# Kernel tuning notes

Measured on AMD Instinct MI355X. Metric: run time of the kernel, lower is better.

## Reference

```python
import jax, jax.numpy as jnp
import numpy as np

NUM_HEADS = 16
HEAD_DIM = 64
D_MODEL = NUM_HEADS * HEAD_DIM  # 1024
FEATURE_DIM = 2 * HEAD_DIM      # 128


def setup_inputs() -> dict:
    key = jax.random.key(0)
    ks = jax.random.split(key, 6)
    B, S = 4, 8192
    scale = D_MODEL ** -0.5
    x = jax.random.normal(ks[0], (B, S, D_MODEL), dtype=jnp.float32)
    Wq = jax.random.normal(ks[1], (D_MODEL, D_MODEL), dtype=jnp.float32) * scale
    Wk = jax.random.normal(ks[2], (D_MODEL, D_MODEL), dtype=jnp.float32) * scale
    Wv = jax.random.normal(ks[3], (D_MODEL, D_MODEL), dtype=jnp.float32) * scale
    Wo = jax.random.normal(ks[4], (D_MODEL, D_MODEL), dtype=jnp.float32) * scale
    # random_features buffer: [head_dim, feature_dim], scaled by head_dim**-0.5
    rf = jax.random.normal(ks[5], (HEAD_DIM, FEATURE_DIM), dtype=jnp.float32) * (HEAD_DIM ** -0.5)
    return {"x": x, "Wq": Wq, "Wk": Wk, "Wv": Wv, "Wo": Wo, "rf": rf}


def _phi(x, rf):
    # x: [B, H, S, head_dim] -> [B, H, S, feature_dim]
    proj = jnp.matmul(x, rf)  # [B, H, S, 2*head_dim]
    cos_p, sin_p = jnp.split(proj, 2, axis=-1)
    return jnp.concatenate([jnp.cos(cos_p), jnp.sin(sin_p)], axis=-1) * (FEATURE_DIM ** -0.5)


def reference(x, Wq, Wk, Wv, Wo, rf):
    B, S, _ = x.shape
    def heads(y):  # [B, S, D] -> [B, H, S, head_dim]
        return y.reshape(B, S, NUM_HEADS, HEAD_DIM).transpose(0, 2, 1, 3)
    Q = heads(x @ Wq)
    K = heads(x @ Wk)
    V = heads(x @ Wv)
    Qp = _phi(Q, rf)  # [B, H, S, F]
    Kp = _phi(K, rf)
    KV = jnp.einsum('bhsf,bhsd->bhfd', Kp, V)        # [B, H, F, head_dim]
    QKV = jnp.einsum('bhsf,bhfd->bhsd', Qp, KV)      # [B, H, S, head_dim]
    Z = jnp.einsum('bhsf,bhf->bhs', Qp, Kp.sum(axis=2))[..., None]
    Z = jnp.clip(Z, 1e-6, None)
    out = (QKV / Z).transpose(0, 2, 1, 3).reshape(B, S, D_MODEL)
    return out @ Wo
```

## Files before the change

### kernel.cpp

```cpp
#include <hip/hip_runtime.h>
#include <stdint.h>


#define DEVINL __device__ __forceinline__

typedef float f32x4 __attribute__((ext_vector_type(4)));
typedef __bf16 bf16x8 __attribute__((ext_vector_type(8)));
typedef unsigned short u16;

#define TSTR 136
#define RSTR 72

DEVINL u16 f2bf(float f) {
  union { float f; uint32_t u; } v; v.f = f;
  uint32_t u = v.u;
  u += 0x7fffu + ((u >> 16) & 1u);
  return (u16)(u >> 16);
}
DEVINL float bf2f(u16 h) {
  union { uint32_t u; float f; } v; v.u = ((uint32_t)h) << 16;
  return v.f;
}

#define GLOAD16(gp, lp) __builtin_amdgcn_global_load_lds( \
    (const __attribute__((address_space(1))) unsigned int*)(gp), \
    (__attribute__((address_space(3))) unsigned int*)(lp), 16, 0, 0)

template <int ROWS>
DEVINL void stage_r128(const uint8_t* g, size_t stride, u16* lds, int wave, int lane) {
#pragma unroll
  for (int j = 0; j < ROWS / 32; ++j) {
    int row = wave * (ROWS / 4) + j * 8 + (lane >> 3);
    GLOAD16(g + (size_t)row * stride + (size_t)(lane & 7) * 16,
            (uint8_t*)lds + (size_t)(wave * (ROWS / 4) + j * 8) * 128);
  }
}
template <int ROWS>
DEVINL void stage_r256(const uint8_t* g, size_t stride, u16* lds, int wave, int lane) {
#pragma unroll
  for (int j = 0; j < ROWS / 16; ++j) {
    int row = wave * (ROWS / 4) + j * 4 + (lane >> 4);
    GLOAD16(g + (size_t)row * stride + (size_t)(lane & 15) * 16,
            (uint8_t*)lds + (size_t)(wave * (ROWS / 4) + j * 4) * 256);
  }
}

DEVINL void stage128_sw(const uint8_t* g, size_t stride, u16* lds, int wave, int lane) {
  const int c = (lane & 7) ^ (lane >> 3);
#pragma unroll
  for (int j = 0; j < 4; ++j) {
    int row = wave * 32 + j * 8 + (lane >> 3);
    GLOAD16(g + (size_t)row * stride + (size_t)c * 16,
            (uint8_t*)lds + (size_t)(wave * 32 + j * 8) * 128);
  }
}

DEVINL void mma128_sw(const u16* As, const u16* Bs, f32x4 acc[4][4],
                      int wr, int wc, int lane) {
#pragma unroll
  for (int kk = 0; kk < 2; ++kk) {
    const int cw = kk * 4 + (lane >> 4);
    const int sw = (cw ^ (lane & 7)) * 8;
    bf16x8 a[4], b[4];
#pragma unroll
    for (int m = 0; m < 4; ++m)
      a[m] = *(const bf16x8*)&As[(size_t)(wr * 64 + m * 16 + (lane & 15)) * 64 + sw];
#pragma unroll
    for (int n = 0; n < 4; ++n)
      b[n] = *(const bf16x8*)&Bs[(size_t)(wc * 64 + n * 16 + (lane & 15)) * 64 + sw];
#pragma unroll
    for (int m = 0; m < 4; ++m)
#pragma unroll
      for (int n = 0; n < 4; ++n)
        acc[m][n] = __builtin_amdgcn_mfma_f32_16x16x32_bf16(a[m], b[n], acc[m][n], 0, 0, 0);
  }
}


__global__ __launch_bounds__(256) void cast_x_kernel(
    const float* __restrict__ src, u16* __restrict__ dst, long n4) {
  long i = (long)blockIdx.x * 256 + threadIdx.x;
  const long stride = (long)gridDim.x * 256;
  const float4* s4 = (const float4*)src;
  uint2* d4 = (uint2*)dst;
  for (; i < n4; i += stride) {
    float4 v = s4[i];
    uint2 o;
    o.x = (uint32_t)f2bf(v.x) | ((uint32_t)f2bf(v.y) << 16);
    o.y = (uint32_t)f2bf(v.z) | ((uint32_t)f2bf(v.w) << 16);
    d4[i] = o;
  }
}

__global__ __launch_bounds__(256) void transpose_cast_kernel(
    const float* __restrict__ src, u16* __restrict__ dst, int R, int C) {
  __shared__ float tile[32 * 33];
  const int ntr = R >> 5;
  const int tr = blockIdx.x % ntr, tc = blockIdx.x / ntr;
  const int tid = threadIdx.x;
  {
    int r = tid >> 3, c4 = (tid & 7) * 4;
    float4 v = *(const float4*)&src[(size_t)(tr * 32 + r) * C + tc * 32 + c4];
    tile[r * 33 + c4 + 0] = v.x;
    tile[r * 33 + c4 + 1] = v.y;
    tile[r * 33 + c4 + 2] = v.z;
    tile[r * 33 + c4 + 3] = v.w;
  }
  __syncthreads();
  {
    int c = tid >> 3, r4 = (tid & 7) * 4;
    uint2 o;
    o.x = (uint32_t)f2bf(tile[(r4 + 0) * 33 + c]) |
          ((uint32_t)f2bf(tile[(r4 + 1) * 33 + c]) << 16);
    o.y = (uint32_t)f2bf(tile[(r4 + 2) * 33 + c]) |
          ((uint32_t)f2bf(tile[(r4 + 3) * 33 + c]) << 16);
    *(uint2*)&dst[(size_t)(tc * 32 + c) * R + tr * 32 + r4] = o;
  }
}

__global__ __launch_bounds__(256, 3) void gemm_qkv_phi_kernel(
    const u16* __restrict__ xb, const u16* __restrict__ wT,
    const u16* __restrict__ rfT,
    u16* __restrict__ Qp, u16* __restrict__ KpT, u16* __restrict__ VhT) {
  __shared__ u16 smem[26624];
  u16* As = smem;
  u16* Bs = smem + 8192;
  u16* Rs = smem + 17408;
  const int tid = threadIdx.x, lane = tid & 63, wave = tid >> 6;
  const int wr = wave >> 1, wc = wave & 1;
  const int xcd = blockIdx.x & 7;
  const int i = blockIdx.x >> 3;
  const int g = i >> 6, j = i & 63;
  const int tn = (g % 3) * 8 + (j >> 3);
  const int tm = xcd * 32 + (g / 3) * 8 + (j & 7);
  const int tensor = tn >> 3;

  f32x4 acc[4][4];
#pragma unroll
  for (int m = 0; m < 4; ++m)
#pragma unroll
    for (int n = 0; n < 4; ++n) acc[m][n] = (f32x4){0.f, 0.f, 0.f, 0.f};

  const uint8_t* aB = (const uint8_t*)(xb + (size_t)tm * 128 * 1024);
  const uint8_t* bB = (const uint8_t*)(wT + (size_t)tn * 128 * 1024);
  for (int kt = 0; kt < 16; ++kt) {
    stage128_sw(aB + kt * 128, 2048, As, wave, lane);
    stage128_sw(bB + kt * 128, 2048, Bs, wave, lane);
    __syncthreads();
    mma128_sw(As, Bs, acc, wr, wc, lane);
    __syncthreads();
  }

  const int b = (tm * 128) >> 13;
  const int sblk = (tm * 128) & 8191;

  if (tensor == 2) {
#pragma unroll
    for (int m = 0; m < 4; ++m) {
      int sl = wr * 64 + m * 16 + (lane >> 4) * 4;
#pragma unroll
      for (int n = 0; n < 4; ++n) {
        int cl = wc * 64 + n * 16 + (lane & 15);
#pragma unroll
        for (int r = 0; r < 4; ++r) smem[cl * TSTR + sl + r] = f2bf(acc[m][n][r]);
      }
    }
    __syncthreads();
#pragma unroll
    for (int it = 0; it < 8; ++it) {
      int cl = it * 16 + (tid >> 4);
      int c = (tn & 7) * 128 + cl;
      int h = c >> 6, d = c & 63;
      size_t off = ((size_t)((b * 16 + h) * 64 + d)) * 8192 + sblk + (tid & 15) * 8;
      *(uint4*)&VhT[off] = *(const uint4*)&smem[cl * TSTR + (tid & 15) * 8];
    }
    return;
  }

#pragma unroll
  for (int m = 0; m < 4; ++m) {
    int sl = wr * 64 + m * 16 + (lane >> 4) * 4;
#pragma unroll
    for (int n = 0; n < 4; ++n) {
      int cl = wc * 64 + n * 16 + (lane & 15);
#pragma unroll
      for (int r = 0; r < 4; ++r) smem[(sl + r) * TSTR + cl] = f2bf(acc[m][n][r]);
    }
  }
#pragma unroll
  for (int p4 = 0; p4 < 4; ++p4) {
    int idx = p4 * 256 + tid;
    int f = idx >> 3, c = idx & 7;
    *(uint4*)&Rs[f * RSTR + c * 8] = *(const uint4*)&rfT[f * 64 + c * 8];
  }
  __syncthreads();

  bf16x8 afr[2][2][2];
#pragma unroll
  for (int hh = 0; hh < 2; ++hh)
#pragma unroll
    for (int kk = 0; kk < 2; ++kk) {
      const int ko = kk * 32 + (lane >> 4) * 8;
#pragma unroll
      for (int m = 0; m < 2; ++m)
        afr[hh][kk][m] = *(const bf16x8*)&smem[
            (size_t)(wave * 32 + m * 16 + (lane & 15)) * TSTR + hh * 64 + ko];
    }
  __syncthreads();

  const float SC = 0.088388347648318447f;
#pragma unroll
  for (int hh = 0; hh < 2; ++hh) {
    const int h = (tn & 7) * 2 + hh;
    f32x4 p[2][8];
#pragma unroll
    for (int m = 0; m < 2; ++m)
#pragma unroll
      for (int n = 0; n < 8; ++n) p[m][n] = (f32x4){0.f, 0.f, 0.f, 0.f};
#pragma unroll
    for (int kk = 0; kk < 2; ++kk) {
      const int ko = kk * 32 + (lane >> 4) * 8;
      bf16x8 bb[8];
#pragma unroll
      for (int n = 0; n < 8; ++n)
        bb[n] = *(const bf16x8*)&Rs[(size_t)(n * 16 + (lane & 15)) * RSTR + ko];
#pragma unroll
      for (int m = 0; m < 2; ++m)
#pragma unroll
        for (int n = 0; n < 8; ++n)
          p[m][n] = __builtin_amdgcn_mfma_f32_16x16x32_bf16(afr[hh][kk][m], bb[n], p[m][n], 0, 0, 0);
    }

    if (tensor == 0) {
#pragma unroll
      for (int m = 0; m < 2; ++m)
#pragma unroll
        for (int n = 0; n < 8; ++n) {
          int f = n * 16 + (lane & 15);
          int sl = wave * 32 + m * 16 + (lane >> 4) * 4;
#pragma unroll
          for (int r = 0; r < 4; ++r) {
            float v = ((n < 4) ? __cosf(p[m][n][r]) : __sinf(p[m][n][r])) * SC;
            smem[(sl + r) * TSTR + f] = f2bf(v);
          }
        }
      __syncthreads();
      const size_t base_bh = (size_t)(b * 16 + h) * 8192;
#pragma unroll
      for (int it = 0; it < 8; ++it) {
        int s = it * 16 + (tid >> 4);
        *(uint4*)&Qp[(base_bh + sblk + s) * 128 + (tid & 15) * 8] =
            *(const uint4*)&smem[s * TSTR + (tid & 15) * 8];
      }
    } else {
#pragma unroll
      for (int m = 0; m < 2; ++m)
#pragma unroll
        for (int n = 0; n < 8; ++n) {
          int f = n * 16 + (lane & 15);
          int sl = wave * 32 + m * 16 + (lane >> 4) * 4;
#pragma unroll
          for (int r = 0; r < 4; ++r) {
            float v = ((n < 4) ? __cosf(p[m][n][r]) : __sinf(p[m][n][r])) * SC;
            smem[f * TSTR + sl + r] = f2bf(v);
          }
        }
      __syncthreads();
#pragma unroll
      for (int it = 0; it < 8; ++it) {
        int f = it * 16 + (tid >> 4);
        *(uint4*)&KpT[((size_t)(b * 16 + h) * 128 + f) * 8192 + sblk + (tid & 15) * 8] =
            *(const uint4*)&smem[f * TSTR + (tid & 15) * 8];
      }
    }
    if (hh == 0) __syncthreads();
  }
}

__global__ __launch_bounds__(256) void kv_partial_kernel(
    const u16* __restrict__ KpT, const u16* __restrict__ VhT,
    float* __restrict__ partial) {
  __shared__ u16 smem2[12288];
  __shared__ float ksmem[256];
  u16* As = smem2;
  u16* Bs = smem2 + 8192;
  const int tid = threadIdx.x, lane = tid & 63, wave = tid >> 6;
  const int bh = blockIdx.x >> 4, ch = blockIdx.x & 15;
  const uint8_t* aB = (const uint8_t*)(KpT + (size_t)bh * 128 * 8192 + ch * 512);
  const uint8_t* bB = (const uint8_t*)(VhT + (size_t)bh * 64 * 8192 + ch * 512);

  f32x4 acc[2][4];
#pragma unroll
  for (int m = 0; m < 2; ++m)
#pragma unroll
    for (int n = 0; n < 4; ++n) acc[m][n] = (f32x4){0.f, 0.f, 0.f, 0.f};
  float ks = 0.f;
  const int fK = tid >> 1, sO = (tid & 1) * 32;

  for (int t = 0; t < 8; ++t) {
    stage_r128<128>(aB + t * 128, 16384, As, wave, lane);
    stage_r128<64>(bB + t * 128, 16384, Bs, wave, lane);
    __syncthreads();
#pragma unroll
    for (int i = 0; i < 4; ++i) {
      uint4 v = *(const uint4*)&As[fK * 64 + sO + i * 8];
      ks += bf2f((u16)(v.x & 0xffff)) + bf2f((u16)(v.x >> 16));
      ks += bf2f((u16)(v.y & 0xffff)) + bf2f((u16)(v.y >> 16));
      ks += bf2f((u16)(v.z & 0xffff)) + bf2f((u16)(v.z >> 16));
      ks += bf2f((u16)(v.w & 0xffff)) + bf2f((u16)(v.w >> 16));
    }
#pragma unroll
    for (int kk = 0; kk < 2; ++kk) {
      const int ko = kk * 32 + (lane >> 4) * 8;
      bf16x8 a[2], bb[4];
#pragma unroll
      for (int m = 0; m < 2; ++m)
        a[m] = *(const bf16x8*)&As[(size_t)(wave * 32 + m * 16 + (lane & 15)) * 64 + ko];
#pragma unroll
      for (int n = 0; n < 4; ++n)
        bb[n] = *(const bf16x8*)&Bs[(size_t)(n * 16 + (lane & 15)) * 64 + ko];
#pragma unroll
      for (int m = 0; m < 2; ++m)
#pragma unroll
        for (int n = 0; n < 4; ++n)
          acc[m][n] = __builtin_amdgcn_mfma_f32_16x16x32_bf16(a[m], bb[n], acc[m][n], 0, 0, 0);
    }
    __syncthreads();
  }

  float* pb = partial + (size_t)blockIdx.x * (128 * 65);
#pragma unroll
  for (int m = 0; m < 2; ++m)
#pragma unroll
    for (int n = 0; n < 4; ++n) {
      int d = n * 16 + (lane & 15);
#pragma unroll
      for (int r = 0; r < 4; ++r) {
        int f = wave * 32 + m * 16 + (lane >> 4) * 4 + r;
        pb[f * 65 + d] = acc[m][n][r];
      }
    }
  ksmem[tid] = ks;
  __syncthreads();
  if (tid < 128) pb[tid * 65 + 64] = ksmem[2 * tid] + ksmem[2 * tid + 1];
}

__global__ __launch_bounds__(256) void kv_reduce_kernel(
    const float* __restrict__ partial, u16* __restrict__ KVT) {
  const int bh = blockIdx.x, tid = threadIdx.x;
  for (int e = tid; e < 8320; e += 256) {
    float s = 0.f;
#pragma unroll
    for (int c = 0; c < 16; ++c) s += partial[(size_t)(bh * 16 + c) * 8320 + e];
    int f = e / 65, col = e % 65;
    KVT[((size_t)bh * 80 + col) * 128 + f] = f2bf(s);
  }
  for (int i = tid; i < 15 * 128; i += 256)
    KVT[((size_t)bh * 80 + 65) * 128 + i] = 0;
}

__global__ __launch_bounds__(256) void qkv_div_kernel(
    const u16* __restrict__ Qp, const u16* __restrict__ KVT, u16* __restrict__ A) {
  __shared__ u16 smem2[26624];
  u16* Qs = smem2;
  u16* Ks = smem2 + 16384;
  const int tid = threadIdx.x, lane = tid & 63, wave = tid >> 6;
  const int bh = blockIdx.x >> 6, st = blockIdx.x & 63;

  stage_r256<128>((const uint8_t*)(Qp + ((size_t)bh * 8192 + st * 128) * 128), 256,
                  Qs, wave, lane);
  stage_r256<80>((const uint8_t*)(KVT + (size_t)bh * 80 * 128), 256, Ks, wave, lane);
  __syncthreads();

  f32x4 acc[2][5];
#pragma unroll
  for (int m = 0; m < 2; ++m)
#pragma unroll
    for (int n = 0; n < 5; ++n) acc[m][n] = (f32x4){0.f, 0.f, 0.f, 0.f};

#pragma unroll
  for (int kk = 0; kk < 4; ++kk) {
    const int ko = kk * 32 + (lane >> 4) * 8;
    bf16x8 a[2], bb[5];
#pragma unroll
    for (int m = 0; m < 2; ++m)
      a[m] = *(const bf16x8*)&Qs[(size_t)(wave * 32 + m * 16 + (lane & 15)) * 128 + ko];
#pragma unroll
    for (int n = 0; n < 5; ++n)
      bb[n] = *(const bf16x8*)&Ks[(size_t)(n * 16 + (lane & 15)) * 128 + ko];
#pragma unroll
    for (int m = 0; m < 2; ++m)
#pragma unroll
      for (int n = 0; n < 5; ++n)
        acc[m][n] = __builtin_amdgcn_mfma_f32_16x16x32_bf16(a[m], bb[n], acc[m][n], 0, 0, 0);
  }

  const int b_ = bh >> 4, h = bh & 15;
#pragma unroll
  for (int m = 0; m < 2; ++m) {
#pragma unroll
    for (int r = 0; r < 4; ++r) {
      float z = fmaxf(__shfl(acc[m][4][r], lane & 48), 1e-6f);
      int srow = st * 128 + wave * 32 + m * 16 + (lane >> 4) * 4 + r;
      size_t rowb = ((size_t)b_ * 8192 + srow) * 1024 + h * 64;
#pragma unroll
      for (int n = 0; n < 4; ++n)
        A[rowb + n * 16 + (lane & 15)] = f2bf(acc[m][n][r] / z);
    }
  }
}

__global__ __launch_bounds__(256, 3) void gemm_out_kernel(
    const u16* __restrict__ A, const u16* __restrict__ WoT, float* __restrict__ out) {
  __shared__ u16 smem[16384];
  u16* As = smem;
  u16* Bs = smem + 8192;
  const int tid = threadIdx.x, lane = tid & 63, wave = tid >> 6;
  const int wr = wave >> 1, wc = wave & 1;
  const int nb = (blockIdx.x & 7) * 256 + (blockIdx.x >> 3);
  const int tn = nb & 7, tm = nb >> 3;

  f32x4 acc[4][4];
#pragma unroll
  for (int m = 0; m < 4; ++m)
#pragma unroll
    for (int n = 0; n < 4; ++n) acc[m][n] = (f32x4){0.f, 0.f, 0.f, 0.f};

  const uint8_t* aB = (const uint8_t*)(A + (size_t)tm * 128 * 1024);
  const uint8_t* bB = (const uint8_t*)(WoT + (size_t)tn * 128 * 1024);
  for (int kt = 0; kt < 16; ++kt) {
    stage128_sw(aB + kt * 128, 2048, As, wave, lane);
    stage128_sw(bB + kt * 128, 2048, Bs, wave, lane);
    __syncthreads();
    mma128_sw(As, Bs, acc, wr, wc, lane);
    __syncthreads();
  }

  const int rowbase = tm * 128 + wr * 64;
  const int colbase = tn * 128 + wc * 64;
#pragma unroll
  for (int m = 0; m < 4; ++m)
#pragma unroll
    for (int n = 0; n < 4; ++n) {
      int col = colbase + n * 16 + (lane & 15);
      int row = rowbase + m * 16 + (lane >> 4) * 4;
#pragma unroll
      for (int r = 0; r < 4; ++r)
        out[(size_t)(row + r) * 1024 + col] = acc[m][n][r];
    }
}


extern "C" void kernel_launch(void* const* d_in, const int* in_sizes, int n_in,
                              void* d_out, int out_size, void* d_ws, size_t ws_size,
                              hipStream_t stream) {
  const float* x  = (const float*)d_in[0];
  const float* Wq = (const float*)d_in[1];
  const float* Wk = (const float*)d_in[2];
  const float* Wv = (const float*)d_in[3];
  const float* Wo = (const float*)d_in[4];
  const float* rf = (const float*)d_in[5];
  float* out = (float*)d_out;

  if (ws_size < (size_t)411058176) return;

  u16* ws = (u16*)d_ws;
  u16* xb    = ws;
  u16* Qp    = ws + 33554432UL;
  u16* KpT   = ws + 100663296UL;
  u16* VhT   = ws + 167772160UL;
  u16* wqkvT = ws + 201326592UL;
  u16* woT   = ws + 204472320UL;
  u16* rfT   = ws + 205520896UL;
  float* partial = (float*)xb;
  u16* KVT   = wqkvT;
  u16* Abuf  = xb;

  cast_x_kernel<<<4096, 256, 0, stream>>>(x, xb, 8388608L);
  transpose_cast_kernel<<<1024, 256, 0, stream>>>(Wq, wqkvT,            1024, 1024);
  transpose_cast_kernel<<<1024, 256, 0, stream>>>(Wk, wqkvT + 1048576,  1024, 1024);
  transpose_cast_kernel<<<1024, 256, 0, stream>>>(Wv, wqkvT + 2097152,  1024, 1024);
  transpose_cast_kernel<<<1024, 256, 0, stream>>>(Wo, woT,              1024, 1024);
  transpose_cast_kernel<<<8,    256, 0, stream>>>(rf, rfT,              64,   128);

  gemm_qkv_phi_kernel<<<6144, 256, 0, stream>>>(xb, wqkvT, rfT, Qp, KpT, VhT);
  kv_partial_kernel<<<1024, 256, 0, stream>>>(KpT, VhT, partial);
  kv_reduce_kernel<<<64, 256, 0, stream>>>(partial, KVT);
  qkv_div_kernel<<<4096, 256, 0, stream>>>(Qp, KVT, Abuf);
  gemm_out_kernel<<<2048, 256, 0, stream>>>(Abuf, woT, out);
}
```

Baseline: 542.1 us.

## Use nontemporal stores, merge weight transposes, widen kv_reduce grid, fuse key-sum into MFMA loads

Most large global writes (bf16 x, Qp, KpT, VhT, final output) become nontemporal stores so streaming data bypasses cache retention. The four weight transpose launches are merged into one kernel, and rf gets its own small kernel. kv_reduce is spread over 512 blocks instead of 64 to use more CUs. kv_partial computes the Kp column sums from the bf16 fragments already loaded for the MFMA, reduced with wave shuffles, instead of doing a separate LDS read pass plus a shared-memory reduction. Nontemporal stores risk evicting data that the next kernel would have read from L2 or MALL, such as Qp and KpT.

```diff
diff --git a/kernel.cpp b/kernel.cpp
--- a/kernel.cpp
+++ b/kernel.cpp
@@ -6,6 +6,8 @@
 
 typedef float f32x4 __attribute__((ext_vector_type(4)));
 typedef __bf16 bf16x8 __attribute__((ext_vector_type(8)));
+typedef uint32_t u32x4 __attribute__((ext_vector_type(4)));
+typedef uint32_t u32x2 __attribute__((ext_vector_type(2)));
 typedef unsigned short u16;
 
 #define TSTR 136
@@ -21,6 +23,12 @@
   union { uint32_t u; float f; } v; v.u = ((uint32_t)h) << 16;
   return v.f;
 }
+DEVINL void nt_store16(u16* p, const u16* s) {
+  __builtin_nontemporal_store(*(const u32x4*)s, (u32x4*)p);
+}
+DEVINL void nt_store8(u16* p, u32x2 v) {
+  __builtin_nontemporal_store(v, (u32x2*)p);
+}
 
 #define GLOAD16(gp, lp) __builtin_amdgcn_global_load_lds( \
     (const __attribute__((address_space(1))) unsigned int*)(gp), \
@@ -82,25 +90,54 @@
   long i = (long)blockIdx.x * 256 + threadIdx.x;
   const long stride = (long)gridDim.x * 256;
   const float4* s4 = (const float4*)src;
-  uint2* d4 = (uint2*)dst;
+  u32x2* d4 = (u32x2*)dst;
   for (; i < n4; i += stride) {
     float4 v = s4[i];
-    uint2 o;
+    u32x2 o;
     o.x = (uint32_t)f2bf(v.x) | ((uint32_t)f2bf(v.y) << 16);
     o.y = (uint32_t)f2bf(v.z) | ((uint32_t)f2bf(v.w) << 16);
-    d4[i] = o;
-  }
-}
-
-__global__ __launch_bounds__(256) void transpose_cast_kernel(
-    const float* __restrict__ src, u16* __restrict__ dst, int R, int C) {
+    __builtin_nontemporal_store(o, &d4[i]);
+  }
+}
+
+__global__ __launch_bounds__(256) void transpose_cast4_kernel(
+    const float* __restrict__ w0, const float* __restrict__ w1,
+    const float* __restrict__ w2, const float* __restrict__ w3,
+    u16* __restrict__ d012, u16* __restrict__ d3) {
   __shared__ float tile[32 * 33];
-  const int ntr = R >> 5;
-  const int tr = blockIdx.x % ntr, tc = blockIdx.x / ntr;
+  const int w = blockIdx.x >> 10, bi = blockIdx.x & 1023;
+  const float* src = (w == 0) ? w0 : (w == 1) ? w1 : (w == 2) ? w2 : w3;
+  u16* dst = (w < 3) ? (d012 + (size_t)w * 1048576) : d3;
+  const int tr = bi & 31, tc = bi >> 5;
   const int tid = threadIdx.x;
   {
     int r = tid >> 3, c4 = (tid & 7) * 4;
-    float4 v = *(const float4*)&src[(size_t)(tr * 32 + r) * C + tc * 32 + c4];
+    float4 v = *(const float4*)&src[(size_t)(tr * 32 + r) * 1024 + tc * 32 + c4];
+    tile[r * 33 + c4 + 0] = v.x;
+    tile[r * 33 + c4 + 1] = v.y;
+    tile[r * 33 + c4 + 2] = v.z;
+    tile[r * 33 + c4 + 3] = v.w;
+  }
+  __syncthreads();
+  {
+    int c = tid >> 3, r4 = (tid & 7) * 4;
+    u32x2 o;
+    o.x = (uint32_t)f2bf(tile[(r4 + 0) * 33 + c]) |
+          ((uint32_t)f2bf(tile[(r4 + 1) * 33 + c]) << 16);
+    o.y = (uint32_t)f2bf(tile[(r4 + 2) * 33 + c]) |
+          ((uint32_t)f2bf(tile[(r4 + 3) * 33 + c]) << 16);
+    nt_store8(&dst[(size_t)(tc * 32 + c) * 1024 + tr * 32 + r4], o);
+  }
+}
+
+__global__ __launch_bounds__(256) void transpose_cast_rf_kernel(
+    const float* __restrict__ src, u16* __restrict__ dst) {
+  __shared__ float tile[32 * 33];
+  const int tr = blockIdx.x & 1, tc = blockIdx.x >> 1;
+  const int tid = threadIdx.x;
+  {
+    int r = tid >> 3, c4 = (tid & 7) * 4;
+    float4 v = *(const float4*)&src[(size_t)(tr * 32 + r) * 128 + tc * 32 + c4];
     tile[r * 33 + c4 + 0] = v.x;
     tile[r * 33 + c4 + 1] = v.y;
     tile[r * 33 + c4 + 2] = v.z;
@@ -114,7 +151,7 @@
           ((uint32_t)f2bf(tile[(r4 + 1) * 33 + c]) << 16);
     o.y = (uint32_t)f2bf(tile[(r4 + 2) * 33 + c]) |
           ((uint32_t)f2bf(tile[(r4 + 3) * 33 + c]) << 16);
-    *(uint2*)&dst[(size_t)(tc * 32 + c) * R + tr * 32 + r4] = o;
+    *(uint2*)&dst[(size_t)(tc * 32 + c) * 64 + tr * 32 + r4] = o;
   }
 }
 
@@ -172,7 +209,7 @@
       int c = (tn & 7) * 128 + cl;
       int h = c >> 6, d = c & 63;
       size_t off = ((size_t)((b * 16 + h) * 64 + d)) * 8192 + sblk + (tid & 15) * 8;
-      *(uint4*)&VhT[off] = *(const uint4*)&smem[cl * TSTR + (tid & 15) * 8];
+      nt_store16(&VhT[off], &smem[cl * TSTR + (tid & 15) * 8]);
     }
     return;
   }
@@ -249,8 +286,8 @@
 #pragma unroll
       for (int it = 0; it < 8; ++it) {
         int s = it * 16 + (tid >> 4);
-        *(uint4*)&Qp[(base_bh + sblk + s) * 128 + (tid & 15) * 8] =
-            *(const uint4*)&smem[s * TSTR + (tid & 15) * 8];
+        nt_store16(&Qp[(base_bh + sblk + s) * 128 + (tid & 15) * 8],
+                   &smem[s * TSTR + (tid & 15) * 8]);
       }
     } else {
 #pragma unroll
@@ -269,8 +306,8 @@
 #pragma unroll
       for (int it = 0; it < 8; ++it) {
         int f = it * 16 + (tid >> 4);
-        *(uint4*)&KpT[((size_t)(b * 16 + h) * 128 + f) * 8192 + sblk + (tid & 15) * 8] =
-            *(const uint4*)&smem[f * TSTR + (tid & 15) * 8];
+        nt_store16(&KpT[((size_t)(b * 16 + h) * 128 + f) * 8192 + sblk + (tid & 15) * 8],
+                   &smem[f * TSTR + (tid & 15) * 8]);
       }
     }
     if (hh == 0) __syncthreads();
@@ -281,7 +318,6 @@
     const u16* __restrict__ KpT, const u16* __restrict__ VhT,
     float* __restrict__ partial) {
   __shared__ u16 smem2[12288];
-  __shared__ float ksmem[256];
   u16* As = smem2;
   u16* Bs = smem2 + 8192;
   const int tid = threadIdx.x, lane = tid & 63, wave = tid >> 6;
@@ -294,28 +330,21 @@
   for (int m = 0; m < 2; ++m)
 #pragma unroll
     for (int n = 0; n < 4; ++n) acc[m][n] = (f32x4){0.f, 0.f, 0.f, 0.f};
-  float ks = 0.f;
-  const int fK = tid >> 1, sO = (tid & 1) * 32;
+  float ks0 = 0.f, ks1 = 0.f;
 
   for (int t = 0; t < 8; ++t) {
     stage_r128<128>(aB + t * 128, 16384, As, wave, lane);
     stage_r128<64>(bB + t * 128, 16384, Bs, wave, lane);
     __syncthreads();
 #pragma unroll
-    for (int i = 0; i < 4; ++i) {
-      uint4 v = *(const uint4*)&As[fK * 64 + sO + i * 8];
-      ks += bf2f((u16)(v.x & 0xffff)) + bf2f((u16)(v.x >> 16));
-      ks += bf2f((u16)(v.y & 0xffff)) + bf2f((u16)(v.y >> 16));
-      ks += bf2f((u16)(v.z & 0xffff)) + bf2f((u16)(v.z >> 16));
-      ks += bf2f((u16)(v.w & 0xffff)) + bf2f((u16)(v.w >> 16));
-    }
-#pragma unroll
     for (int kk = 0; kk < 2; ++kk) {
       const int ko = kk * 32 + (lane >> 4) * 8;
       bf16x8 a[2], bb[4];
 #pragma unroll
       for (int m = 0; m < 2; ++m)
         a[m] = *(const bf16x8*)&As[(size_t)(wave * 32 + m * 16 + (lane & 15)) * 64 + ko];
+#pragma unroll
+      for (int e = 0; e < 8; ++e) { ks0 += (float)a[0][e]; ks1 += (float)a[1][e]; }
 #pragma unroll
       for (int n = 0; n < 4; ++n)
         bb[n] = *(const bf16x8*)&Bs[(size_t)(n * 16 + (lane & 15)) * 64 + ko];
@@ -340,23 +369,28 @@
         pb[f * 65 + d] = acc[m][n][r];
       }
     }
-  ksmem[tid] = ks;
-  __syncthreads();
-  if (tid < 128) pb[tid * 65 + 64] = ksmem[2 * tid] + ksmem[2 * tid + 1];
+  ks0 += __shfl_xor(ks0, 16); ks0 += __shfl_xor(ks0, 32);
+  ks1 += __shfl_xor(ks1, 16); ks1 += __shfl_xor(ks1, 32);
+  if ((lane >> 4) == 0) {
+    pb[(wave * 32 + (lane & 15)) * 65 + 64] = ks0;
+    pb[(wave * 32 + 16 + (lane & 15)) * 65 + 64] = ks1;
+  }
 }
 
 __global__ __launch_bounds__(256) void kv_reduce_kernel(
     const float* __restrict__ partial, u16* __restrict__ KVT) {
-  const int bh = blockIdx.x, tid = threadIdx.x;
-  for (int e = tid; e < 8320; e += 256) {
+  const int bh = blockIdx.x >> 3, eo = (blockIdx.x & 7) * 1040;
+  const int tid = threadIdx.x;
+  for (int e = eo + tid; e < eo + 1040; e += 256) {
     float s = 0.f;
 #pragma unroll
     for (int c = 0; c < 16; ++c) s += partial[(size_t)(bh * 16 + c) * 8320 + e];
     int f = e / 65, col = e % 65;
     KVT[((size_t)bh * 80 + col) * 128 + f] = f2bf(s);
   }
-  for (int i = tid; i < 15 * 128; i += 256)
-    KVT[((size_t)bh * 80 + 65) * 128 + i] = 0;
+  if ((blockIdx.x & 7) == 7)
+    for (int i = tid; i < 15 * 128; i += 256)
+      KVT[((size_t)bh * 80 + 65) * 128 + i] = 0;
 }
 
 __global__ __launch_bounds__(256) void qkv_div_kernel(
@@ -446,7 +480,7 @@
       int row = rowbase + m * 16 + (lane >> 4) * 4;
 #pragma unroll
       for (int r = 0; r < 4; ++r)
-        out[(size_t)(row + r) * 1024 + col] = acc[m][n][r];
+        __builtin_nontemporal_store(acc[m][n][r], &out[(size_t)(row + r) * 1024 + col]);
     }
 }
 
@@ -477,15 +511,12 @@
   u16* Abuf  = xb;
 
   cast_x_kernel<<<4096, 256, 0, stream>>>(x, xb, 8388608L);
-  transpose_cast_kernel<<<1024, 256, 0, stream>>>(Wq, wqkvT,            1024, 1024);
-  transpose_cast_kernel<<<1024, 256, 0, stream>>>(Wk, wqkvT + 1048576,  1024, 1024);
-  transpose_cast_kernel<<<1024, 256, 0, stream>>>(Wv, wqkvT + 2097152,  1024, 1024);
-  transpose_cast_kernel<<<1024, 256, 0, stream>>>(Wo, woT,              1024, 1024);
-  transpose_cast_kernel<<<8,    256, 0, stream>>>(rf, rfT,              64,   128);
+  transpose_cast4_kernel<<<4096, 256, 0, stream>>>(Wq, Wk, Wv, Wo, wqkvT, woT);
+  transpose_cast_rf_kernel<<<8, 256, 0, stream>>>(rf, rfT);
 
   gemm_qkv_phi_kernel<<<6144, 256, 0, stream>>>(xb, wqkvT, rfT, Qp, KpT, VhT);
   kv_partial_kernel<<<1024, 256, 0, stream>>>(KpT, VhT, partial);
-  kv_reduce_kernel<<<64, 256, 0, stream>>>(partial, KVT);
+  kv_reduce_kernel<<<512, 256, 0, stream>>>(partial, KVT);
   qkv_div_kernel<<<4096, 256, 0, stream>>>(Qp, KVT, Abuf);
   gemm_out_kernel<<<2048, 256, 0, stream>>>(Abuf, woT, out);
 }
```

Result: faster. 525.2 us (-3.1%).
